# Kernel optimization log

Hardware: AMD Instinct MI355X
Metric: run time of the kernel (lower is better)

Reference implementation:

```python
import jax, jax.numpy as jnp
import numpy as np
from jax import lax

# Module config (from init_kwargs)
PADDING = (1, 1)
DILATION = (1, 1)
GROUPS = 1
# stride param is initialized to ones(2); effective integer stride = floor(stride) = (1, 1).
# Output shape depends on this value, so it must be static under jit.
INT_STRIDE = (1, 1)


def setup_inputs() -> dict:
    key = jax.random.key(0)
    k1, k2 = jax.random.split(key)
    B, Cin, H, W = 32, 128, 64, 64
    Cout, kH, kW = 256, 3, 3
    x = jax.random.normal(k1, (B, Cin, H, W), dtype=jnp.float32)
    # reset_parameters: uniform(-stdv, stdv), stdv = 1/sqrt(Cin*kH*kW)
    stdv = 1.0 / np.sqrt(Cin * kH * kW)
    weight = jax.random.uniform(k2, (Cout, Cin // GROUPS, kH, kW), dtype=jnp.float32,
                                minval=-stdv, maxval=stdv)
    stride = jnp.ones((2,), dtype=jnp.float32)
    return {"x": x, "weight": weight, "stride": stride}


def reference(x, weight, stride):
    # Integer strides = floor(stride); with stride initialized to ones this is (1, 1).
    # (Static under jit; floor has zero derivative a.e., so stride only affects
    #  sampling locations, exactly as in the CUDA im2col forward.)
    out = lax.conv_general_dilated(
        x, weight,
        window_strides=INT_STRIDE,
        padding=[(PADDING[0], PADDING[0]), (PADDING[1], PADDING[1])],
        rhs_dilation=DILATION,
        dimension_numbers=("NCHW", "OIHW", "NCHW"),
        feature_group_count=GROUPS,
    )
    return out
```

## Files before the change

kernel.cpp:

```cpp
#include <hip/hip_runtime.h>

typedef __attribute__((ext_vector_type(8))) short short8;
typedef __attribute__((ext_vector_type(4))) float f32x4;

#define XP_ELEMS (32u * 66u * 66u * 128u)
#define WT_ELEMS (256u * 1152u)
#define WS_NEED  ((size_t)(XP_ELEMS + WT_ELEMS) * 2u)

typedef const __attribute__((address_space(1))) void* gp1_t;
typedef __attribute__((address_space(3))) void* lp3_t;

__device__ __forceinline__ void gload16(const void* g, void* l) {
  __builtin_amdgcn_global_load_lds((gp1_t)g, (lp3_t)l, 16, 0, 0);
}

__device__ __forceinline__ short f2bf(float f) {
  unsigned u = __float_as_uint(f);
  u = (u + 0x7FFFu + ((u >> 16) & 1u)) >> 16;
  return (short)u;
}

__global__ __launch_bounds__(256) void prepass_x(const float* __restrict__ x,
                                                 short* __restrict__ xp) {
  __shared__ short lds[64 * 128];
  const int y = blockIdx.x;
  const int b = blockIdx.y;
  const int t = threadIdx.x;

  const float* src = x + (long)b * 128 * 4096 + y * 64;
#pragma unroll
  for (int i = 0; i < 8; ++i) {
    int f4 = t + i * 256;
    int cin = f4 >> 4, px4 = f4 & 15;
    float4 v = *(const float4*)(src + (long)cin * 4096 + px4 * 4);
    float vv[4] = {v.x, v.y, v.z, v.w};
#pragma unroll
    for (int j = 0; j < 4; ++j) {
      int px = px4 * 4 + j;
      int g = (cin >> 3) ^ ((px ^ (px >> 2)) & 15);
      lds[px * 128 + (g << 3) + (cin & 7)] = f2bf(vv[j]);
    }
  }
  __syncthreads();
  short* dst = xp + ((long)(b * 66 + y + 1) * 66 + 1) * 128;
#pragma unroll
  for (int i = 0; i < 4; ++i) {
    int f8 = t + i * 256;
    int px = f8 >> 4, c8 = f8 & 15;
    int g = c8 ^ ((px ^ (px >> 2)) & 15);
    short8 v = *(const short8*)&lds[px * 128 + (g << 3)];
    *(short8*)(dst + (long)px * 128 + c8 * 8) = v;
  }
  short8 z = (short8)0;
  short* rowbase = xp + (long)(b * 66 + y + 1) * 66 * 128;
  if (t < 32) {
    int px = (t < 16) ? 0 : 65;
    int c8 = t & 15;
    *(short8*)(rowbase + (long)px * 128 + c8 * 8) = z;
  }
  if (y == 0) {
    short* r0 = xp + (long)(b * 66) * 66 * 128;
    for (int idx = t; idx < 66 * 16; idx += 256) *(short8*)(r0 + idx * 8) = z;
  }
  if (y == 63) {
    short* r65 = xp + ((long)(b * 66) + 65) * 66 * 128;
    for (int idx = t; idx < 66 * 16; idx += 256) *(short8*)(r65 + idx * 8) = z;
  }
}

__global__ __launch_bounds__(256) void prepass_w(const float* __restrict__ w,
                                                 short* __restrict__ wt) {
  int o    = blockIdx.x * 256 + threadIdx.x;
  int cout = o / 1152;
  int r    = o % 1152;
  int kh   = r / 384;
  int kw   = (r / 128) % 3;
  int cin  = r & 127;
  wt[o] = f2bf(w[((cout * 128 + cin) * 3 + kh) * 3 + kw]);
}

__global__ __launch_bounds__(512, 2) void conv_gemm(const short* __restrict__ xp,
                                                    const short* __restrict__ wt,
                                                    float* __restrict__ out) {
  __shared__ alignas(16) short Al[4][256 * 32];
  __shared__ alignas(16) short Bl[4][256 * 32];
  const int tid = threadIdx.x;
  const int w   = tid >> 6;
  const int l   = tid & 63;
  const int l15 = l & 15;
  const int q   = l >> 4;
  const int wm2 = w >> 2;
  const int wn4 = w & 3;
  const int ntile = blockIdx.x;

  const int r0  = tid >> 2;
  const int r1  = r0 + 128;
  const int p0  = tid & 3;
  const int cs0 = p0 ^ ((r0 >> 1) & 3);
  const int cs1 = p0 ^ ((r1 >> 1) & 3);
  const long aoff0 = (long)r0 * 1152 + (cs0 << 3);
  const long aoff1 = (long)r1 * 1152 + (cs1 << 3);

  long boff0, boff1;
  {
    int n0 = (ntile << 8) + r0;
    int bb = n0 >> 12, yx = n0 & 4095, y = yx >> 6, xx = yx & 63;
    boff0 = ((long)(bb * 66 + y) * 66 + xx) * 128 + (cs0 << 3);
    int n1 = n0 + 128;
    bb = n1 >> 12; yx = n1 & 4095; y = yx >> 6; xx = yx & 63;
    boff1 = ((long)(bb * 66 + y) * 66 + xx) * 128 + (cs1 << 3);
  }
  const int ldst0 = tid * 8;
  const int ldst1 = (512 + tid) * 8;

  int aRd[8], bRd[4];
#pragma unroll
  for (int mi = 0; mi < 8; ++mi) {
    int r = (wm2 << 7) + (mi << 4) + l15;
    aRd[mi] = r * 32 + ((q ^ ((r >> 1) & 3)) << 3);
  }
#pragma unroll
  for (int nj = 0; nj < 4; ++nj) {
    int r = (wn4 << 6) + (nj << 4) + l15;
    bRd[nj] = r * 32 + ((q ^ ((r >> 1) & 3)) << 3);
  }

  f32x4 acc[8][4];
#pragma unroll
  for (int mi = 0; mi < 8; ++mi)
#pragma unroll
    for (int nj = 0; nj < 4; ++nj) acc[mi][nj] = (f32x4)0.f;

  auto STAGE = [&](int kss, int bufS) {
    const int kq = kss >> 2;
    const int kh = kq / 3, kw2 = kq % 3;
    const long sBs = (long)(kh * 66 + kw2) * 128 + ((kss & 3) << 5);
    const long ka  = (long)kss << 5;
    gload16(wt + aoff0 + ka, &Al[bufS][ldst0]);
    gload16(wt + aoff1 + ka, &Al[bufS][ldst1]);
    gload16(xp + boff0 + sBs, &Bl[bufS][ldst0]);
    gload16(xp + boff1 + sBs, &Bl[bufS][ldst1]);
  };

  STAGE(0, 0); STAGE(1, 1); STAGE(2, 2);
  asm volatile("s_waitcnt vmcnt(8)" ::: "memory");
  __builtin_amdgcn_s_barrier();
  __builtin_amdgcn_sched_barrier(0);

#pragma unroll
  for (int ks = 0; ks < 36; ++ks) {
    if (ks + 3 < 36) STAGE(ks + 3, (ks + 3) & 3);

    const short* Ab = &Al[ks & 3][0];
    const short* Bb = &Bl[ks & 3][0];
    short8 af[8], bf[4];
#pragma unroll
    for (int mi = 0; mi < 8; ++mi) af[mi] = *(const short8*)&Ab[aRd[mi]];
#pragma unroll
    for (int nj = 0; nj < 4; ++nj) bf[nj] = *(const short8*)&Bb[bRd[nj]];

    __builtin_amdgcn_s_setprio(1);
#pragma unroll
    for (int mi = 0; mi < 8; ++mi)
#pragma unroll
      for (int nj = 0; nj < 4; ++nj)
        acc[mi][nj] = __builtin_amdgcn_mfma_f32_16x16x32_bf16(af[mi], bf[nj],
                                                              acc[mi][nj], 0, 0, 0);
    __builtin_amdgcn_s_setprio(0);

    if (ks + 1 < 36) {
      if (ks + 3 < 36)      asm volatile("s_waitcnt vmcnt(8)" ::: "memory");
      else if (ks + 2 < 36) asm volatile("s_waitcnt vmcnt(4)" ::: "memory");
      else                  asm volatile("s_waitcnt vmcnt(0)" ::: "memory");
      __builtin_amdgcn_s_barrier();
      __builtin_amdgcn_sched_barrier(0);
    }
  }

  const int bimg = ntile >> 4;
  const int yx0  = ((ntile & 15) << 8) + (wn4 << 6) + l15;
  float* outb = out + (long)bimg * (256 * 4096) + yx0;
#pragma unroll
  for (int mi = 0; mi < 8; ++mi) {
#pragma unroll
    for (int r = 0; r < 4; ++r) {
      const int cout = (wm2 << 7) + (mi << 4) + (q << 2) + r;
      float* orow = outb + (long)cout * 4096;
#pragma unroll
      for (int nj = 0; nj < 4; ++nj) orow[nj << 4] = acc[mi][nj][r];
    }
  }
}

__global__ __launch_bounds__(256) void naive_conv(const float* __restrict__ x,
                                                  const float* __restrict__ wgt,
                                                  float* __restrict__ out) {
  long o = (long)blockIdx.x * 256 + threadIdx.x;
  int xx = (int)(o & 63);
  int y  = (int)((o >> 6) & 63);
  int co = (int)((o >> 12) & 255);
  int b  = (int)(o >> 20);
  float s = 0.f;
  for (int ci = 0; ci < 128; ++ci) {
    for (int kh = 0; kh < 3; ++kh) {
      int iy = y + kh - 1;
      if (iy < 0 || iy > 63) continue;
      for (int kw = 0; kw < 3; ++kw) {
        int ix = xx + kw - 1;
        if (ix < 0 || ix > 63) continue;
        s += x[((long)(b * 128 + ci) * 64 + iy) * 64 + ix] *
             wgt[((co * 128 + ci) * 3 + kh) * 3 + kw];
      }
    }
  }
  out[o] = s;
}

extern "C" void kernel_launch(void* const* d_in, const int* in_sizes, int n_in,
                              void* d_out, int out_size, void* d_ws, size_t ws_size,
                              hipStream_t stream) {
  (void)in_sizes; (void)n_in;
  const float* x   = (const float*)d_in[0];
  const float* wgt = (const float*)d_in[1];
  float* out = (float*)d_out;
  if (ws_size >= WS_NEED) {
    short* xp = (short*)d_ws;
    short* wt = xp + XP_ELEMS;
    prepass_x<<<dim3(64, 32), dim3(256), 0, stream>>>(x, xp);
    prepass_w<<<dim3(WT_ELEMS / 256), dim3(256), 0, stream>>>(wgt, wt);
    conv_gemm<<<dim3(512), dim3(512), 0, stream>>>(xp, wt, out);
  } else {
    naive_conv<<<dim3(out_size / 256), dim3(256), 0, stream>>>(x, wgt, out);
  }
}
```

Before: 258.3 us.

## Restructure conv GEMM main loop into 8-phase ping-pong schedule with K=64 stages

Replaces the 4-buffer K=32 pipeline with a 2-stage K=64 LDS double buffer split into half-tiles. Each iteration is broken into eight phases, each interleaving a global-to-LDS load of one quarter tile, fragment loads, and a quarter of the MFMAs, with barriers between phases. The goal is to spread memory traffic and LDS reads evenly across MFMA work and halve the number of K iterations. The cost is many more barriers per K step and more intricate index and waitcnt bookkeeping, which could stall warps or introduce ordering bugs.

```diff
diff --git a/kernel.cpp b/kernel.cpp
--- a/kernel.cpp
+++ b/kernel.cpp
@@ -82,8 +82,8 @@
 __global__ __launch_bounds__(512, 2) void conv_gemm(const short* __restrict__ xp,
                                                     const short* __restrict__ wt,
                                                     float* __restrict__ out) {
-  __shared__ alignas(16) short Al[4][256 * 32];
-  __shared__ alignas(16) short Bl[4][256 * 32];
+  __shared__ alignas(16) short Alds[2 * 2 * 2 * 128 * 32];
+  __shared__ alignas(16) short Blds[2 * 2 * 2 * 128 * 32];
   const int tid = threadIdx.x;
   const int w   = tid >> 6;
   const int l   = tid & 63;
@@ -93,37 +93,37 @@
   const int wn4 = w & 3;
   const int ntile = blockIdx.x;
 
-  const int r0  = tid >> 2;
-  const int r1  = r0 + 128;
-  const int p0  = tid & 3;
-  const int cs0 = p0 ^ ((r0 >> 1) & 3);
-  const int cs1 = p0 ^ ((r1 >> 1) & 3);
-  const long aoff0 = (long)r0 * 1152 + (cs0 << 3);
-  const long aoff1 = (long)r1 * 1152 + (cs1 << 3);
-
-  long boff0, boff1;
-  {
-    int n0 = (ntile << 8) + r0;
-    int bb = n0 >> 12, yx = n0 & 4095, y = yx >> 6, xx = yx & 63;
-    boff0 = ((long)(bb * 66 + y) * 66 + xx) * 128 + (cs0 << 3);
-    int n1 = n0 + 128;
-    bb = n1 >> 12; yx = n1 & 4095; y = yx >> 6; xx = yx & 63;
-    boff1 = ((long)(bb * 66 + y) * 66 + xx) * 128 + (cs1 << 3);
-  }
-  const int ldst0 = tid * 8;
-  const int ldst1 = (512 + tid) * 8;
+  const int r6 = (tid >> 2) & 63;
+  const int cc = tid >> 8;
+  const int pp = tid & 3;
+  const int cs = pp ^ ((r6 >> 1) & 3);
+  const int aTh  = r6 * 1152 + cc * 32 + cs * 8;
+  const int ldsA = cc * 4096 + r6 * 32 + pp * 8;
+  const int ldsB0 = ldsA + ((r6 & 32) << 5);
+  int bTh[2][2];
+#pragma unroll
+  for (int hb = 0; hb < 2; ++hb)
+#pragma unroll
+    for (int nq = 0; nq < 2; ++nq) {
+      int R  = (r6 & 31) + ((r6 >> 5) << 6) + nq * 32;
+      int n  = (ntile << 8) + (hb << 7) + R;
+      int bb = n >> 12, yy = (n >> 6) & 63, xx = n & 63;
+      bTh[hb][nq] = ((bb * 66 + yy) * 66 + xx) * 128 + cc * 32 + cs * 8;
+    }
 
   int aRd[8], bRd[4];
 #pragma unroll
   for (int mi = 0; mi < 8; ++mi) {
-    int r = (wm2 << 7) + (mi << 4) + l15;
+    int r = (mi << 4) + l15;
     aRd[mi] = r * 32 + ((q ^ ((r >> 1) & 3)) << 3);
   }
 #pragma unroll
   for (int nj = 0; nj < 4; ++nj) {
-    int r = (wn4 << 6) + (nj << 4) + l15;
+    int r = ((wn4 & 1) << 6) + (nj << 4) + l15;
     bRd[nj] = r * 32 + ((q ^ ((r >> 1) & 3)) << 3);
   }
+  const int aHB = wm2 * 8192;
+  const int bHB = (wn4 >> 1) * 8192;
 
   f32x4 acc[8][4];
 #pragma unroll
@@ -131,50 +131,101 @@
 #pragma unroll
     for (int nj = 0; nj < 4; ++nj) acc[mi][nj] = (f32x4)0.f;
 
-  auto STAGE = [&](int kss, int bufS) {
-    const int kq = kss >> 2;
-    const int kh = kq / 3, kw2 = kq % 3;
-    const long sBs = (long)(kh * 66 + kw2) * 128 + ((kss & 3) << 5);
-    const long ka  = (long)kss << 5;
-    gload16(wt + aoff0 + ka, &Al[bufS][ldst0]);
-    gload16(wt + aoff1 + ka, &Al[bufS][ldst1]);
-    gload16(xp + boff0 + sBs, &Bl[bufS][ldst0]);
-    gload16(xp + boff1 + sBs, &Bl[bufS][ldst1]);
-  };
-
-  STAGE(0, 0); STAGE(1, 1); STAGE(2, 2);
-  asm volatile("s_waitcnt vmcnt(8)" ::: "memory");
-  __builtin_amdgcn_s_barrier();
-  __builtin_amdgcn_sched_barrier(0);
-
-#pragma unroll
-  for (int ks = 0; ks < 36; ++ks) {
-    if (ks + 3 < 36) STAGE(ks + 3, (ks + 3) & 3);
-
-    const short* Ab = &Al[ks & 3][0];
-    const short* Bb = &Bl[ks & 3][0];
-    short8 af[8], bf[4];
-#pragma unroll
-    for (int mi = 0; mi < 8; ++mi) af[mi] = *(const short8*)&Ab[aRd[mi]];
-#pragma unroll
-    for (int nj = 0; nj < 4; ++nj) bf[nj] = *(const short8*)&Bb[bRd[nj]];
-
+  short8 af[4][2], bf[4][2];
+
+  auto ST_A = [&](int s, int v, int kb) {
+    gload16(wt + kb + v * 73728 + aTh,
+            &Alds[s * 16384 + v * 2048 + ldsA]);
+    gload16(wt + kb + 147456 + v * 73728 + aTh,
+            &Alds[s * 16384 + 8192 + v * 2048 + ldsA]);
+  };
+  auto ST_B = [&](int s, int nq, int sh) {
+    gload16(xp + sh + bTh[0][nq], &Blds[s * 16384 + (nq << 10) + ldsB0]);
+    gload16(xp + sh + bTh[1][nq], &Blds[s * 16384 + 8192 + (nq << 10) + ldsB0]);
+  };
+  auto LD_A = [&](int s, int mq) {
+#pragma unroll
+    for (int i = 0; i < 4; ++i)
+#pragma unroll
+      for (int c = 0; c < 2; ++c)
+        af[i][c] = *(const short8*)&Alds[s * 16384 + aHB + c * 4096 + aRd[mq * 4 + i]];
+  };
+  auto LD_B = [&](int s, int nq) {
+#pragma unroll
+    for (int j = 0; j < 2; ++j)
+#pragma unroll
+      for (int c = 0; c < 2; ++c)
+        bf[nq * 2 + j][c] =
+            *(const short8*)&Blds[s * 16384 + bHB + c * 4096 + bRd[nq * 2 + j]];
+  };
+  auto MM = [&](int mq, int nq) {
     __builtin_amdgcn_s_setprio(1);
 #pragma unroll
-    for (int mi = 0; mi < 8; ++mi)
-#pragma unroll
-      for (int nj = 0; nj < 4; ++nj)
-        acc[mi][nj] = __builtin_amdgcn_mfma_f32_16x16x32_bf16(af[mi], bf[nj],
-                                                              acc[mi][nj], 0, 0, 0);
+    for (int c = 0; c < 2; ++c)
+#pragma unroll
+      for (int i = 0; i < 4; ++i)
+#pragma unroll
+        for (int j = 0; j < 2; ++j)
+          acc[mq * 4 + i][nq * 2 + j] = __builtin_amdgcn_mfma_f32_16x16x32_bf16(
+              af[i][c], bf[nq * 2 + j][c], acc[mq * 4 + i][nq * 2 + j], 0, 0, 0);
     __builtin_amdgcn_s_setprio(0);
-
-    if (ks + 1 < 36) {
-      if (ks + 3 < 36)      asm volatile("s_waitcnt vmcnt(8)" ::: "memory");
-      else if (ks + 2 < 36) asm volatile("s_waitcnt vmcnt(4)" ::: "memory");
-      else                  asm volatile("s_waitcnt vmcnt(0)" ::: "memory");
-      __builtin_amdgcn_s_barrier();
-      __builtin_amdgcn_sched_barrier(0);
-    }
+  };
+
+#define BAR()   __builtin_amdgcn_s_barrier()
+#define SBAR()  __builtin_amdgcn_sched_barrier(0)
+#define LGKM0() do { asm volatile("s_waitcnt lgkmcnt(0)" ::: "memory"); SBAR(); } while (0)
+#define VMC(n)  asm volatile("s_waitcnt vmcnt(" #n ")" ::: "memory")
+
+  ST_A(0, 0, 0);  ST_B(0, 0, 0);
+  ST_A(0, 1, 0);  ST_B(0, 1, 0);
+  ST_A(1, 0, 64); ST_B(1, 0, 64);
+  VMC(4);
+  BAR(); SBAR();
+
+#pragma unroll
+  for (int J = 0; J < 9; ++J) {
+    const int kh  = J / 3,        kw  = J % 3;
+    const int khn = (J + 1) / 3,  kwn = (J + 1) % 3;
+    const int kb1 = J * 128 + 64;
+    const int kb2 = (J + 1) * 128;
+    const int sh1 = (kh * 66 + kw) * 128 + 64;
+    const int sh2 = (khn * 66 + kwn) * 128;
+    const int sh3 = sh2 + 64;
+
+    LD_A(0, 0); LD_B(0, 0);
+    ST_A(1, 1, kb1);
+    asm volatile("s_waitcnt lgkmcnt(8)" ::: "memory");
+    BAR(); LGKM0(); MM(0, 0); BAR(); SBAR();
+
+    LD_B(0, 1);
+    ST_B(1, 1, sh1);
+    BAR(); LGKM0(); MM(0, 1); BAR(); SBAR();
+
+    LD_A(0, 1);
+    if (J < 8) ST_A(0, 0, kb2);
+    BAR(); LGKM0(); MM(1, 0); BAR(); SBAR();
+
+    if (J < 8) ST_B(0, 0, sh2);
+    BAR(); LGKM0(); MM(1, 1);
+    if (J < 8) { VMC(4); } else { VMC(0); }
+    BAR(); SBAR();
+
+    LD_A(1, 0); LD_B(1, 0);
+    if (J < 8) ST_A(0, 1, kb2);
+    asm volatile("s_waitcnt lgkmcnt(8)" ::: "memory");
+    BAR(); LGKM0(); MM(0, 0); BAR(); SBAR();
+
+    LD_B(1, 1);
+    if (J < 8) ST_B(0, 1, sh2);
+    BAR(); LGKM0(); MM(0, 1); BAR(); SBAR();
+
+    LD_A(1, 1);
+    if (J < 8) ST_A(1, 0, kb2 + 64);
+    BAR(); LGKM0(); MM(1, 0); BAR(); SBAR();
+
+    if (J < 8) ST_B(1, 0, sh3);
+    BAR(); LGKM0(); MM(1, 1);
+    if (J < 8) { VMC(4); BAR(); SBAR(); }
   }
 
   const int bimg = ntile >> 4;
@@ -190,6 +241,10 @@
       for (int nj = 0; nj < 4; ++nj) orow[nj << 4] = acc[mi][nj][r];
     }
   }
+#undef BAR
+#undef SBAR
+#undef LGKM0
+#undef VMC
 }
 
 __global__ __launch_bounds__(256) void naive_conv(const float* __restrict__ x,
```

Result: no change. 254.4 us (-1.5%).
